# Optimization experiments

Measured on AMD Instinct MI355X. Metric: run time of the kernel, lower is better.

Reference implementation:

```python
import jax, jax.numpy as jnp
import numpy as np

V_PER_MESH = 6596
HIDDEN = 128
# per-body-part clamp limits from the original module (parts 1..14)
LIMITS = jnp.array([0.04, 0.06, 0.04, 0.04, 0.02, 0.02, 0.04, 0.04,
                    0.03, 0.03, 0.02, 0.02, 0.01, 0.01], dtype=jnp.float32)


def setup_inputs() -> dict:
    key = jax.random.key(0)
    ks = jax.random.split(key, 16)
    B, V, H = 32, V_PER_MESH, HIDDEN
    N = B * V
    E = 3 * N
    inp = {}
    inp["verts"] = jax.random.normal(ks[0], (N, 3), jnp.float32)
    inp["normals"] = jax.random.normal(ks[1], (N, 3), jnp.float32)
    inp["anchor_v"] = jax.random.uniform(ks[2], (V, 3), jnp.float32)
    inp["edges"] = jax.random.randint(ks[3], (E, 2), 0, N)
    inp["part_id"] = jax.random.randint(ks[4], (V,), 0, 14)
    dims = [3, H + 3, H + 3]  # first gconv sees only vert normals (vert_feat_dim=0)
    i = 5
    for l, d in enumerate(dims):
        s = 1.0 / np.sqrt(d)
        inp[f"w0_{l}"] = jax.random.normal(ks[i], (d, H), jnp.float32) * s; i += 1
        inp[f"b0_{l}"] = jnp.zeros((H,), jnp.float32)
        inp[f"w1_{l}"] = jax.random.normal(ks[i], (d, H), jnp.float32) * s; i += 1
        inp[f"b1_{l}"] = jnp.zeros((H,), jnp.float32)
    inp["w_off"] = jax.random.normal(ks[i], (H + 3, 3), jnp.float32) * 0.01
    inp["b_off"] = jnp.zeros((3,), jnp.float32)
    return inp


def _forward(verts, normals, anchor_v, edges, part_id, layers, w_off, b_off):
    N = verts.shape[0]
    B = N // V_PER_MESH
    e0, e1 = edges[:, 0], edges[:, 1]
    feats = normals  # vert_pos_packed (verts_normals_packed), vert_feats=None
    for (w0, b0, w1, b1) in layers:
        x0 = feats @ w0 + b0            # [N,H] self transform
        x1 = feats @ w1 + b1            # [N,H] neighbor transform
        # undirected gather-scatter over mesh edges
        nbr = jnp.zeros_like(x0).at[e0].add(x1[e1]).at[e1].add(x1[e0])
        h = jax.nn.relu(x0 + nbr)       # vert_feats_nopos
        feats = jnp.concatenate([h, normals], axis=1)  # [N,H+3]
    deform = jnp.tanh(feats @ w_off + b_off)  # [N,3]
    # per-body-part clamp, vectorized: one limit per vertex, tiled over meshes
    lim = jnp.tile(LIMITS[part_id], B)[:, None]          # [N,1]
    clamped = jnp.clip(deform, -lim, lim)
    anchor = jnp.tile(anchor_v, (B, 1))                  # [N,3]
    new_verts = verts + clamped * anchor                 # offset_verts
    return new_verts, h


def reference(verts, normals, anchor_v, edges, part_id,
              w0_0, b0_0, w1_0, b1_0,
              w0_1, b0_1, w1_1, b1_1,
              w0_2, b0_2, w1_2, b1_2,
              w_off, b_off):
    layers = [(w0_0, b0_0, w1_0, b1_0),
              (w0_1, b0_1, w1_1, b1_1),
              (w0_2, b0_2, w1_2, b1_2)]
    return _forward(verts, normals, anchor_v, edges, part_id, layers, w_off, b_off)
```

## Files before the change

### kernel.cpp

```cpp
#include <hip/hip_runtime.h>

#define N_TOT 211072
#define V_MESH 6596
#define E_TOT 633216
#define CAP 32
#define KP 184
#define KSTEPS 5

typedef __attribute__((ext_vector_type(8))) short bf16x8;
typedef __attribute__((ext_vector_type(4))) float f32x4;

__constant__ float c_LIM[14] = {0.04f,0.06f,0.04f,0.04f,0.02f,0.02f,0.04f,0.04f,
                                0.03f,0.03f,0.02f,0.02f,0.01f,0.01f};

__device__ __forceinline__ unsigned f2bf(float f) {
    unsigned x = __float_as_uint(f);
    return (x + 0x7fffu + ((x >> 16) & 1u)) >> 16;
}
__device__ __forceinline__ float bflo(unsigned u) { return __uint_as_float(u << 16); }
__device__ __forceinline__ float bfhi(unsigned u) { return __uint_as_float(u & 0xffff0000u); }

__global__ __launch_bounds__(256) void init_adj_kernel(int4* __restrict__ adj4) {
    size_t idx = (size_t)blockIdx.x * 256 + threadIdx.x;
    adj4[idx] = make_int4(N_TOT, N_TOT, N_TOT, N_TOT);
}

__global__ __launch_bounds__(256) void fill_adj_kernel(const int* __restrict__ edges,
                                                       int* __restrict__ cnt,
                                                       int* __restrict__ adj) {
    int e = blockIdx.x * 256 + threadIdx.x;
    if (e >= E_TOT) return;
    int2 ed = ((const int2*)edges)[e];
    int p0 = atomicAdd(&cnt[ed.x], 1);
    if (p0 < CAP) adj[(size_t)ed.x * CAP + p0] = ed.y;
    int p1 = atomicAdd(&cnt[ed.y], 1);
    if (p1 < CAP) adj[(size_t)ed.y * CAP + p1] = ed.x;
}

__global__ __launch_bounds__(256) void conv_w_kernel(const float* __restrict__ w0,
                                                     const float* __restrict__ b0,
                                                     const float* __restrict__ w1,
                                                     const float* __restrict__ b1,
                                                     short* __restrict__ Wt,
                                                     float* __restrict__ bb) {
    int c = blockIdx.x;
    int k = threadIdx.x;
    const float* w = (c < 128) ? w0 : w1;
    int cc = c & 127;
    if (k < KP) {
        unsigned val = (k < 131) ? f2bf(w[(size_t)k * 128 + cc]) : 0u;
        Wt[(size_t)c * KP + k] = (short)val;
    }
    if (k == 0) bb[c] = (c < 128) ? b0[cc] : b1[cc];
}

__global__ __launch_bounds__(256) void mm3_kernel(const float* __restrict__ normals,
                                                  const float* __restrict__ w0,
                                                  const float* __restrict__ b0,
                                                  const float* __restrict__ w1,
                                                  const float* __restrict__ b1,
                                                  unsigned* __restrict__ xc) {
    __shared__ float nL[32][3];
    int t = threadIdx.x;
    int row0 = blockIdx.x * 32;
    if (t < 96) {
        int r = t / 3, k = t - r * 3;
        nL[r][k] = normals[(size_t)(row0 + r) * 3 + k];
    }
    __syncthreads();
    int m  = (t >> 6) & 1;
    int rh = t >> 7;
    int c2 = t & 63;
    const float* w = m ? w1 : w0;
    const float* b = m ? b1 : b0;
    float wA0 = w[0*128 + 2*c2],     wA1 = w[1*128 + 2*c2],     wA2 = w[2*128 + 2*c2];
    float wB0 = w[0*128 + 2*c2 + 1], wB1 = w[1*128 + 2*c2 + 1], wB2 = w[2*128 + 2*c2 + 1];
    float bA = b[2*c2], bB = b[2*c2 + 1];
    #pragma unroll
    for (int r = 0; r < 16; ++r) {
        int lr = rh * 16 + r;
        float vA = bA + nL[lr][0]*wA0 + nL[lr][1]*wA1 + nL[lr][2]*wA2;
        float vB = bB + nL[lr][0]*wB0 + nL[lr][1]*wB1 + nL[lr][2]*wB2;
        xc[(size_t)(row0 + lr) * 128 + m * 64 + c2] = f2bf(vA) | (f2bf(vB) << 16);
    }
}

__global__ __launch_bounds__(1024, 8) void fused_kernel(const unsigned* __restrict__ xc_in,
                                                        const float* __restrict__ normals,
                                                        const int* __restrict__ cnt,
                                                        const int* __restrict__ adj,
                                                        const short* __restrict__ Wt,
                                                        const float* __restrict__ bb,
                                                        unsigned* __restrict__ xc_out) {
    __shared__ short tileA[16 * KP];
    __shared__ short tileC[16 * 256];
    int tid  = threadIdx.x;
    int w    = tid >> 6;
    int lane = tid & 63;
    int g    = lane >> 4;
    int ln   = lane & 15;
    int row0 = blockIdx.x * 16;
    int i    = row0 + w;

    int deg0 = cnt[i];
    int jv = (lane < CAP) ? adj[(size_t)i * CAP + lane] : (int)N_TOT;
    unsigned selfu = xc_in[(size_t)i * 128 + lane];
    float nv = (lane < 3) ? normals[(size_t)i * 3 + lane] : 0.f;
    int cb = w * 16;
    float bv = bb[cb + ln];
    bf16x8 bfrag[KSTEPS];
    #pragma unroll
    for (int kk = 0; kk < KSTEPS; ++kk)
        bfrag[kk] = *(const bf16x8*)(Wt + (size_t)(cb + ln) * KP + kk * 32 + g * 8);

    const unsigned* x1b = xc_in + 64 + lane;
    unsigned u[8];
    #pragma unroll
    for (int q = 0; q < 8; ++q) {
        int j = __builtin_amdgcn_readlane(jv, q);
        u[q] = x1b[(size_t)j * 128];
    }
    float a0 = bflo(selfu), a1 = bfhi(selfu);
    float d0 = 0.f, d1 = 0.f;
    #pragma unroll
    for (int q = 0; q < 8; q += 2) {
        a0 += bflo(u[q]);     a1 += bfhi(u[q]);
        d0 += bflo(u[q + 1]); d1 += bfhi(u[q + 1]);
    }
    int deg = (deg0 > CAP) ? CAP : deg0;
    deg = __builtin_amdgcn_readfirstlane(deg);
    for (int base = 8; base < deg; base += 8) {
        unsigned v[8];
        #pragma unroll
        for (int q = 0; q < 8; ++q) {
            int j = __builtin_amdgcn_readlane(jv, base + q);
            v[q] = x1b[(size_t)j * 128];
        }
        #pragma unroll
        for (int q = 0; q < 8; q += 2) {
            a0 += bflo(v[q]);     a1 += bfhi(v[q]);
            d0 += bflo(v[q + 1]); d1 += bfhi(v[q + 1]);
        }
    }
    a0 = fmaxf(a0 + d0, 0.f);
    a1 = fmaxf(a1 + d1, 0.f);

    ((unsigned*)tileA)[w * (KP / 2) + lane] = f2bf(a0) | (f2bf(a1) << 16);
    unsigned nb = f2bf(nv);
    unsigned nb0 = __shfl((int)nb, 0), nb1 = __shfl((int)nb, 1), nb2 = __shfl((int)nb, 2);
    if (lane < 16) {
        unsigned v = (lane == 0) ? (nb0 | (nb1 << 16)) : (lane == 1) ? nb2 : 0u;
        ((unsigned*)tileA)[w * (KP / 2) + 64 + lane] = v;
    }
    __syncthreads();

    f32x4 acc = {bv, bv, bv, bv};
    #pragma unroll
    for (int kk = 0; kk < KSTEPS; ++kk) {
        bf16x8 af = *(const bf16x8*)(tileA + ln * KP + kk * 32 + g * 8);
        acc = __builtin_amdgcn_mfma_f32_16x16x32_bf16(af, bfrag[kk], acc, 0, 0, 0);
    }
    #pragma unroll
    for (int j = 0; j < 4; ++j) {
        float po = __shfl_xor(acc[j], 1);
        if (!(ln & 1)) {
            unsigned pk = f2bf(acc[j]) | (f2bf(po) << 16);
            int d = w * 8 + (ln >> 1);
            int row = g * 4 + j;
            ((unsigned*)tileC)[row * 128 + (d ^ (g << 3))] = pk;
        }
    }
    __syncthreads();

    int key = (w >> 2) << 3;
    ushort4 v4 = *(const ushort4*)&((unsigned*)tileC)[w * 128 + ((2 * lane) ^ key)];
    ((ushort4*)(xc_out + (size_t)(row0 + w) * 128))[lane] = v4;
}

__global__ __launch_bounds__(256) void final_fused_kernel(const unsigned* __restrict__ xc_in,
                                                          const int* __restrict__ cnt,
                                                          const int* __restrict__ adj,
                                                          const float* __restrict__ normals,
                                                          const float* __restrict__ verts,
                                                          const float* __restrict__ anchor_v,
                                                          const int* __restrict__ part_id,
                                                          const float* __restrict__ w_off,
                                                          const float* __restrict__ b_off,
                                                          float* __restrict__ hout,
                                                          float* __restrict__ out_verts) {
    __shared__ float wo[131 * 3];
    for (int t = threadIdx.x; t < 131 * 3; t += 256) wo[t] = w_off[t];
    __syncthreads();
    int tid  = threadIdx.x;
    int w    = tid >> 6;
    int lane = tid & 63;
    int i    = blockIdx.x * 4 + w;

    int deg0 = cnt[i];
    int jv = (lane < CAP) ? adj[(size_t)i * CAP + lane] : (int)N_TOT;
    unsigned selfu = xc_in[(size_t)i * 128 + lane];

    const unsigned* x1b = xc_in + 64 + lane;
    unsigned u[8];
    #pragma unroll
    for (int q = 0; q < 8; ++q) {
        int j = __builtin_amdgcn_readlane(jv, q);
        u[q] = x1b[(size_t)j * 128];
    }
    float a0 = bflo(selfu), a1 = bfhi(selfu);
    float d0 = 0.f, d1 = 0.f;
    #pragma unroll
    for (int q = 0; q < 8; q += 2) {
        a0 += bflo(u[q]);     a1 += bfhi(u[q]);
        d0 += bflo(u[q + 1]); d1 += bfhi(u[q + 1]);
    }
    int deg = (deg0 > CAP) ? CAP : deg0;
    deg = __builtin_amdgcn_readfirstlane(deg);
    for (int base = 8; base < deg; base += 8) {
        unsigned v[8];
        #pragma unroll
        for (int q = 0; q < 8; ++q) {
            int j = __builtin_amdgcn_readlane(jv, base + q);
            v[q] = x1b[(size_t)j * 128];
        }
        #pragma unroll
        for (int q = 0; q < 8; q += 2) {
            a0 += bflo(v[q]);     a1 += bfhi(v[q]);
            d0 += bflo(v[q + 1]); d1 += bfhi(v[q + 1]);
        }
    }
    a0 = fmaxf(a0 + d0, 0.f);
    a1 = fmaxf(a1 + d1, 0.f);

    float2 hv; hv.x = a0; hv.y = a1;
    ((float2*)(hout + (size_t)i * 128))[lane] = hv;

    int cA = 2 * lane, cB = 2 * lane + 1;
    float s0 = a0 * wo[cA * 3 + 0] + a1 * wo[cB * 3 + 0];
    float s1 = a0 * wo[cA * 3 + 1] + a1 * wo[cB * 3 + 1];
    float s2 = a0 * wo[cA * 3 + 2] + a1 * wo[cB * 3 + 2];
    #pragma unroll
    for (int d = 32; d; d >>= 1) {
        s0 += __shfl_xor(s0, d);
        s1 += __shfl_xor(s1, d);
        s2 += __shfl_xor(s2, d);
    }
    if (lane < 3) {
        int v = i % V_MESH;
        float n0 = normals[(size_t)i * 3 + 0];
        float n1 = normals[(size_t)i * 3 + 1];
        float n2 = normals[(size_t)i * 3 + 2];
        float s = (lane == 0) ? s0 : (lane == 1) ? s1 : s2;
        s += n0 * wo[128 * 3 + lane] + n1 * wo[129 * 3 + lane] + n2 * wo[130 * 3 + lane];
        s += b_off[lane];
        float dd = tanhf(s);
        float lim = c_LIM[part_id[v]];
        dd = fminf(fmaxf(dd, -lim), lim);
        out_verts[(size_t)i * 3 + lane] =
            verts[(size_t)i * 3 + lane] + dd * anchor_v[(size_t)v * 3 + lane];
    }
}

extern "C" void kernel_launch(void* const* d_in, const int* in_sizes, int n_in,
                              void* d_out, int out_size, void* d_ws, size_t ws_size,
                              hipStream_t stream) {
    const float* verts    = (const float*)d_in[0];
    const float* normals  = (const float*)d_in[1];
    const float* anchor_v = (const float*)d_in[2];
    const int*   edges    = (const int*)d_in[3];
    const int*   part_id  = (const int*)d_in[4];
    const float* w0_0 = (const float*)d_in[5];
    const float* b0_0 = (const float*)d_in[6];
    const float* w1_0 = (const float*)d_in[7];
    const float* b1_0 = (const float*)d_in[8];
    const float* w0_1 = (const float*)d_in[9];
    const float* b0_1 = (const float*)d_in[10];
    const float* w1_1 = (const float*)d_in[11];
    const float* b1_1 = (const float*)d_in[12];
    const float* w0_2 = (const float*)d_in[13];
    const float* b0_2 = (const float*)d_in[14];
    const float* w1_2 = (const float*)d_in[15];
    const float* b1_2 = (const float*)d_in[16];
    const float* w_off = (const float*)d_in[17];
    const float* b_off = (const float*)d_in[18];

    float* out_verts = (float*)d_out;
    float* hout = (float*)d_out + (size_t)3 * N_TOT;

    unsigned* xcB = (unsigned*)d_out;

    char* p = (char*)d_ws;
    unsigned* xcA = (unsigned*)p;  p += (size_t)(N_TOT + 1) * 128 * 4;
    int*   cnt = (int*)p;          p += (size_t)N_TOT * 4;
    int*   adj = (int*)p;          p += (size_t)N_TOT * CAP * 4;
    short* Wt1 = (short*)p;        p += 256 * KP * 2;
    float* bb1 = (float*)p;        p += 256 * 4;
    short* Wt2 = (short*)p;        p += 256 * KP * 2;
    float* bb2 = (float*)p;

    hipMemsetAsync(cnt, 0, (size_t)N_TOT * 4, stream);
    hipMemsetAsync(xcA + (size_t)N_TOT * 128, 0, 512, stream);
    hipMemsetAsync(xcB + (size_t)N_TOT * 128, 0, 512, stream);
    init_adj_kernel<<<N_TOT * CAP / 1024, 256, 0, stream>>>((int4*)adj);
    fill_adj_kernel<<<(E_TOT + 255) / 256, 256, 0, stream>>>(edges, cnt, adj);
    conv_w_kernel<<<256, 256, 0, stream>>>(w0_1, b0_1, w1_1, b1_1, Wt1, bb1);
    conv_w_kernel<<<256, 256, 0, stream>>>(w0_2, b0_2, w1_2, b1_2, Wt2, bb2);

    mm3_kernel<<<N_TOT / 32, 256, 0, stream>>>(normals, w0_0, b0_0, w1_0, b1_0, xcA);
    fused_kernel<<<N_TOT / 16, 1024, 0, stream>>>(xcA, normals, cnt, adj, Wt1, bb1, xcB);
    fused_kernel<<<N_TOT / 16, 1024, 0, stream>>>(xcB, normals, cnt, adj, Wt2, bb2, xcA);
    final_fused_kernel<<<N_TOT / 4, 256, 0, stream>>>(xcA, cnt, adj, normals, verts,
                                                      anchor_v, part_id, w_off, b_off,
                                                      hout, out_verts);
}
```

Before: 466.7 us.

## Split wave into halves for 8-byte neighbor gathers and pad adjacency lazily

```diff
diff --git a/kernel.cpp b/kernel.cpp
--- a/kernel.cpp
+++ b/kernel.cpp
@@ -19,10 +19,8 @@
 }
 __device__ __forceinline__ float bflo(unsigned u) { return __uint_as_float(u << 16); }
 __device__ __forceinline__ float bfhi(unsigned u) { return __uint_as_float(u & 0xffff0000u); }
-
-__global__ __launch_bounds__(256) void init_adj_kernel(int4* __restrict__ adj4) {
-    size_t idx = (size_t)blockIdx.x * 256 + threadIdx.x;
-    adj4[idx] = make_int4(N_TOT, N_TOT, N_TOT, N_TOT);
+__device__ __forceinline__ unsigned pk_trunc(float a0, float a1) {
+    return __builtin_amdgcn_perm(__float_as_uint(a1), __float_as_uint(a0), 0x07060302u);
 }
 
 __global__ __launch_bounds__(256) void fill_adj_kernel(const int* __restrict__ edges,
@@ -35,6 +33,16 @@
     if (p0 < CAP) adj[(size_t)ed.x * CAP + p0] = ed.y;
     int p1 = atomicAdd(&cnt[ed.y], 1);
     if (p1 < CAP) adj[(size_t)ed.y * CAP + p1] = ed.x;
+}
+
+__global__ __launch_bounds__(256) void pad_adj_kernel(const int* __restrict__ cnt,
+                                                      int* __restrict__ adj) {
+    int i = blockIdx.x * 256 + threadIdx.x;
+    if (i >= N_TOT) return;
+    int deg = cnt[i]; if (deg > CAP) deg = CAP;
+    int end = (deg <= 8) ? 8 : ((deg + 7) & ~7);
+    if (end > CAP) end = CAP;
+    for (int k = deg; k < end; ++k) adj[(size_t)i * CAP + k] = N_TOT;
 }
 
 __global__ __launch_bounds__(256) void conv_w_kernel(const float* __restrict__ w0,
@@ -97,6 +105,8 @@
     int tid  = threadIdx.x;
     int w    = tid >> 6;
     int lane = tid & 63;
+    int half = lane >> 5;
+    int c    = lane & 31;
     int g    = lane >> 4;
     int ln   = lane & 15;
     int row0 = blockIdx.x * 16;
@@ -104,70 +114,77 @@
 
     int deg0 = cnt[i];
     int jv = (lane < CAP) ? adj[(size_t)i * CAP + lane] : (int)N_TOT;
-    unsigned selfu = xc_in[(size_t)i * 128 + lane];
+    uint2 selfu = *(const uint2*)(xc_in + (size_t)i * 128 + 2 * c);
     float nv = (lane < 3) ? normals[(size_t)i * 3 + lane] : 0.f;
+
+    const unsigned* gbase = xc_in + 64 + 2 * c;
+    uint2 u[4];
+    #pragma unroll
+    for (int q = 0; q < 4; ++q) {
+        int j = __shfl(jv, 2 * q + half);
+        u[q] = *(const uint2*)(gbase + (size_t)j * 128);
+    }
+    float a0 = 0.f, a1 = 0.f, a2 = 0.f, a3 = 0.f;
+    #pragma unroll
+    for (int q = 0; q < 4; ++q) {
+        a0 += bflo(u[q].x); a1 += bfhi(u[q].x);
+        a2 += bflo(u[q].y); a3 += bfhi(u[q].y);
+    }
+    int deg = (deg0 > CAP) ? CAP : deg0;
+    deg = __builtin_amdgcn_readfirstlane(deg);
+    for (int bq = 8; bq < deg; bq += 8) {
+        uint2 v[4];
+        #pragma unroll
+        for (int q = 0; q < 4; ++q) {
+            int j = __shfl(jv, bq + 2 * q + half);
+            v[q] = *(const uint2*)(gbase + (size_t)j * 128);
+        }
+        #pragma unroll
+        for (int q = 0; q < 4; ++q) {
+            a0 += bflo(v[q].x); a1 += bfhi(v[q].x);
+            a2 += bflo(v[q].y); a3 += bfhi(v[q].y);
+        }
+    }
+    a0 += __shfl_xor(a0, 32);
+    a1 += __shfl_xor(a1, 32);
+    a2 += __shfl_xor(a2, 32);
+    a3 += __shfl_xor(a3, 32);
+    a0 = fmaxf(a0 + bflo(selfu.x), 0.f);
+    a1 = fmaxf(a1 + bfhi(selfu.x), 0.f);
+    a2 = fmaxf(a2 + bflo(selfu.y), 0.f);
+    a3 = fmaxf(a3 + bfhi(selfu.y), 0.f);
+
+    unsigned* tA32 = (unsigned*)tileA;
+    unsigned nb = f2bf(nv);
+    unsigned nb0 = __shfl((int)nb, 0), nb1 = __shfl((int)nb, 1), nb2 = __shfl((int)nb, 2);
+    if (half == 0) {
+        uint2 pk;
+        pk.x = pk_trunc(a0, a1);
+        pk.y = pk_trunc(a2, a3);
+        *(uint2*)(tA32 + w * (KP / 2) + 2 * c) = pk;
+    } else if (c < 16) {
+        unsigned v = (c == 0) ? (nb0 | (nb1 << 16)) : (c == 1) ? nb2 : 0u;
+        tA32[w * (KP / 2) + 64 + c] = v;
+    }
+    __syncthreads();
+
     int cb = w * 16;
     float bv = bb[cb + ln];
-    bf16x8 bfrag[KSTEPS];
-    #pragma unroll
-    for (int kk = 0; kk < KSTEPS; ++kk)
-        bfrag[kk] = *(const bf16x8*)(Wt + (size_t)(cb + ln) * KP + kk * 32 + g * 8);
-
-    const unsigned* x1b = xc_in + 64 + lane;
-    unsigned u[8];
-    #pragma unroll
-    for (int q = 0; q < 8; ++q) {
-        int j = __builtin_amdgcn_readlane(jv, q);
-        u[q] = x1b[(size_t)j * 128];
-    }
-    float a0 = bflo(selfu), a1 = bfhi(selfu);
-    float d0 = 0.f, d1 = 0.f;
-    #pragma unroll
-    for (int q = 0; q < 8; q += 2) {
-        a0 += bflo(u[q]);     a1 += bfhi(u[q]);
-        d0 += bflo(u[q + 1]); d1 += bfhi(u[q + 1]);
-    }
-    int deg = (deg0 > CAP) ? CAP : deg0;
-    deg = __builtin_amdgcn_readfirstlane(deg);
-    for (int base = 8; base < deg; base += 8) {
-        unsigned v[8];
-        #pragma unroll
-        for (int q = 0; q < 8; ++q) {
-            int j = __builtin_amdgcn_readlane(jv, base + q);
-            v[q] = x1b[(size_t)j * 128];
-        }
-        #pragma unroll
-        for (int q = 0; q < 8; q += 2) {
-            a0 += bflo(v[q]);     a1 += bfhi(v[q]);
-            d0 += bflo(v[q + 1]); d1 += bfhi(v[q + 1]);
-        }
-    }
-    a0 = fmaxf(a0 + d0, 0.f);
-    a1 = fmaxf(a1 + d1, 0.f);
-
-    ((unsigned*)tileA)[w * (KP / 2) + lane] = f2bf(a0) | (f2bf(a1) << 16);
-    unsigned nb = f2bf(nv);
-    unsigned nb0 = __shfl((int)nb, 0), nb1 = __shfl((int)nb, 1), nb2 = __shfl((int)nb, 2);
-    if (lane < 16) {
-        unsigned v = (lane == 0) ? (nb0 | (nb1 << 16)) : (lane == 1) ? nb2 : 0u;
-        ((unsigned*)tileA)[w * (KP / 2) + 64 + lane] = v;
-    }
-    __syncthreads();
-
     f32x4 acc = {bv, bv, bv, bv};
     #pragma unroll
     for (int kk = 0; kk < KSTEPS; ++kk) {
+        bf16x8 bf = *(const bf16x8*)(Wt + (size_t)(cb + ln) * KP + kk * 32 + g * 8);
         bf16x8 af = *(const bf16x8*)(tileA + ln * KP + kk * 32 + g * 8);
-        acc = __builtin_amdgcn_mfma_f32_16x16x32_bf16(af, bfrag[kk], acc, 0, 0, 0);
+        acc = __builtin_amdgcn_mfma_f32_16x16x32_bf16(af, bf, acc, 0, 0, 0);
     }
     #pragma unroll
     for (int j = 0; j < 4; ++j) {
         float po = __shfl_xor(acc[j], 1);
         if (!(ln & 1)) {
             unsigned pk = f2bf(acc[j]) | (f2bf(po) << 16);
-            int d = w * 8 + (ln >> 1);
+            int dd = w * 8 + (ln >> 1);
             int row = g * 4 + j;
-            ((unsigned*)tileC)[row * 128 + (d ^ (g << 3))] = pk;
+            ((unsigned*)tileC)[row * 128 + (dd ^ (g << 3))] = pk;
         }
     }
     __syncthreads();
@@ -194,53 +211,62 @@
     int tid  = threadIdx.x;
     int w    = tid >> 6;
     int lane = tid & 63;
+    int half = lane >> 5;
+    int c    = lane & 31;
     int i    = blockIdx.x * 4 + w;
 
     int deg0 = cnt[i];
     int jv = (lane < CAP) ? adj[(size_t)i * CAP + lane] : (int)N_TOT;
-    unsigned selfu = xc_in[(size_t)i * 128 + lane];
-
-    const unsigned* x1b = xc_in + 64 + lane;
-    unsigned u[8];
-    #pragma unroll
-    for (int q = 0; q < 8; ++q) {
-        int j = __builtin_amdgcn_readlane(jv, q);
-        u[q] = x1b[(size_t)j * 128];
-    }
-    float a0 = bflo(selfu), a1 = bfhi(selfu);
-    float d0 = 0.f, d1 = 0.f;
-    #pragma unroll
-    for (int q = 0; q < 8; q += 2) {
-        a0 += bflo(u[q]);     a1 += bfhi(u[q]);
-        d0 += bflo(u[q + 1]); d1 += bfhi(u[q + 1]);
+    uint2 selfu = *(const uint2*)(xc_in + (size_t)i * 128 + 2 * c);
+
+    const unsigned* gbase = xc_in + 64 + 2 * c;
+    uint2 u[4];
+    #pragma unroll
+    for (int q = 0; q < 4; ++q) {
+        int j = __shfl(jv, 2 * q + half);
+        u[q] = *(const uint2*)(gbase + (size_t)j * 128);
+    }
+    float a0 = 0.f, a1 = 0.f, a2 = 0.f, a3 = 0.f;
+    #pragma unroll
+    for (int q = 0; q < 4; ++q) {
+        a0 += bflo(u[q].x); a1 += bfhi(u[q].x);
+        a2 += bflo(u[q].y); a3 += bfhi(u[q].y);
     }
     int deg = (deg0 > CAP) ? CAP : deg0;
     deg = __builtin_amdgcn_readfirstlane(deg);
-    for (int base = 8; base < deg; base += 8) {
-        unsigned v[8];
+    for (int bq = 8; bq < deg; bq += 8) {
+        uint2 v[4];
         #pragma unroll
-        for (int q = 0; q < 8; ++q) {
-            int j = __builtin_amdgcn_readlane(jv, base + q);
-            v[q] = x1b[(size_t)j * 128];
+        for (int q = 0; q < 4; ++q) {
+            int j = __shfl(jv, bq + 2 * q + half);
+            v[q] = *(const uint2*)(gbase + (size_t)j * 128);
         }
         #pragma unroll
-        for (int q = 0; q < 8; q += 2) {
-            a0 += bflo(v[q]);     a1 += bfhi(v[q]);
-            d0 += bflo(v[q + 1]); d1 += bfhi(v[q + 1]);
-        }
-    }
-    a0 = fmaxf(a0 + d0, 0.f);
-    a1 = fmaxf(a1 + d1, 0.f);
-
-    float2 hv; hv.x = a0; hv.y = a1;
-    ((float2*)(hout + (size_t)i * 128))[lane] = hv;
-
-    int cA = 2 * lane, cB = 2 * lane + 1;
-    float s0 = a0 * wo[cA * 3 + 0] + a1 * wo[cB * 3 + 0];
-    float s1 = a0 * wo[cA * 3 + 1] + a1 * wo[cB * 3 + 1];
-    float s2 = a0 * wo[cA * 3 + 2] + a1 * wo[cB * 3 + 2];
-    #pragma unroll
-    for (int d = 32; d; d >>= 1) {
+        for (int q = 0; q < 4; ++q) {
+            a0 += bflo(v[q].x); a1 += bfhi(v[q].x);
+            a2 += bflo(v[q].y); a3 += bfhi(v[q].y);
+        }
+    }
+    a0 += __shfl_xor(a0, 32);
+    a1 += __shfl_xor(a1, 32);
+    a2 += __shfl_xor(a2, 32);
+    a3 += __shfl_xor(a3, 32);
+    a0 = fmaxf(a0 + bflo(selfu.x), 0.f);
+    a1 = fmaxf(a1 + bfhi(selfu.x), 0.f);
+    a2 = fmaxf(a2 + bflo(selfu.y), 0.f);
+    a3 = fmaxf(a3 + bfhi(selfu.y), 0.f);
+
+    if (half == 0) {
+        float4 hv; hv.x = a0; hv.y = a1; hv.z = a2; hv.w = a3;
+        *(float4*)(hout + (size_t)i * 128 + 4 * c) = hv;
+    }
+
+    int c4 = 4 * c;
+    float s0 = a0*wo[c4*3+0] + a1*wo[(c4+1)*3+0] + a2*wo[(c4+2)*3+0] + a3*wo[(c4+3)*3+0];
+    float s1 = a0*wo[c4*3+1] + a1*wo[(c4+1)*3+1] + a2*wo[(c4+2)*3+1] + a3*wo[(c4+3)*3+1];
+    float s2 = a0*wo[c4*3+2] + a1*wo[(c4+1)*3+2] + a2*wo[(c4+2)*3+2] + a3*wo[(c4+3)*3+2];
+    #pragma unroll
+    for (int d = 1; d < 32; d <<= 1) {
         s0 += __shfl_xor(s0, d);
         s1 += __shfl_xor(s1, d);
         s2 += __shfl_xor(s2, d);
@@ -301,8 +327,8 @@
     hipMemsetAsync(cnt, 0, (size_t)N_TOT * 4, stream);
     hipMemsetAsync(xcA + (size_t)N_TOT * 128, 0, 512, stream);
     hipMemsetAsync(xcB + (size_t)N_TOT * 128, 0, 512, stream);
-    init_adj_kernel<<<N_TOT * CAP / 1024, 256, 0, stream>>>((int4*)adj);
     fill_adj_kernel<<<(E_TOT + 255) / 256, 256, 0, stream>>>(edges, cnt, adj);
+    pad_adj_kernel<<<(N_TOT + 255) / 256, 256, 0, stream>>>(cnt, adj);
     conv_w_kernel<<<256, 256, 0, stream>>>(w0_1, b0_1, w1_1, b1_1, Wt1, bb1);
     conv_w_kernel<<<256, 256, 0, stream>>>(w0_2, b0_2, w1_2, b1_2, Wt2, bb2);
 
```

Measured after the change: 514.3 us. +10.2%, slower.
